# Optimization experiments

Measured on AMD Instinct MI355X. Metric: run time of the kernel, lower is better.

Reference implementation:

```python
import jax, jax.numpy as jnp
import numpy as np

DILATIONS = (1, 2, 4, 8, 16, 32, 64, 128, 256)
R = 128          # residual/skip channels
K = 3            # kernel size
B, CIN, T = 8, 1, 16384
COUT = 1
L = len(DILATIONS)


def causal_conv(x, w, b, dilation):
    # x: [B, Cin, T], w: [Cout, Cin, K] -> [B, Cout, T], left-padded (causal)
    k = w.shape[-1]
    pad = dilation * (k - 1)
    y = jax.lax.conv_general_dilated(
        x, w, window_strides=(1,), padding=[(pad, 0)],
        rhs_dilation=(dilation,), dimension_numbers=("NCH", "OIH", "NCH"))
    return y + b[None, :, None]


def setup_inputs() -> dict:
    key = jax.random.key(0)
    ks = jax.random.split(key, 11)
    s = 0.1  # weight scale to keep gated activations in a healthy range
    return {
        "x": jax.random.normal(ks[0], (B, CIN, T), jnp.float32),
        "input_w": s * jax.random.normal(ks[1], (R, CIN, 1), jnp.float32),
        "input_b": s * jax.random.normal(ks[2], (R,), jnp.float32),
        "conv_w": s * jax.random.normal(ks[3], (L, 2 * R, R, K), jnp.float32),
        "conv_b": s * jax.random.normal(ks[4], (L, 2 * R), jnp.float32),
        "out_w": s * jax.random.normal(ks[5], (L, R, R, 1), jnp.float32),
        "out_b": s * jax.random.normal(ks[6], (L, R), jnp.float32),
        "output1_w": s * jax.random.normal(ks[7], (R, R * L, 1), jnp.float32),
        "output1_b": s * jax.random.normal(ks[8], (R,), jnp.float32),
        "output2_w": s * jax.random.normal(ks[9], (COUT, R, 1), jnp.float32),
        "output2_b": s * jax.random.normal(ks[10], (COUT,), jnp.float32),
    }


def reference(x, input_w, input_b, conv_w, conv_b, out_w, out_b,
              output1_w, output1_b, output2_w, output2_b):
    # input layer: 1x1 conv + tanh (use_output_transform=False)
    h = jnp.tanh(causal_conv(x, input_w, input_b, 1))

    skips = []
    for i, d in enumerate(DILATIONS):
        pre = causal_conv(h, conv_w[i], conv_b[i], d)      # [B, 2R, T]
        t, g = jnp.split(pre, 2, axis=1)
        z = jnp.tanh(t) * jax.nn.sigmoid(g)                # gated activation
        skips.append(z)                                     # skip = activation out
        res = causal_conv(z, out_w[i], out_b[i], 1)         # 1x1 output transform
        h = h + res                                         # residual connection

    sk = jnp.concatenate(skips, axis=1)                     # [B, R*L, T]
    y = jnp.tanh(causal_conv(sk, output1_w, output1_b, 1))
    out = causal_conv(y, output2_w, output2_b, 1)           # linear
    return out
```

## Files before the change

kernel.cpp:

```cpp
#include <hip/hip_runtime.h>
#include <cstdint>
#include <cstddef>

#define T_LEN 16384
#define BATCH 8
#define NLAYER 9

typedef _Float16 f16;
typedef __attribute__((ext_vector_type(8))) _Float16 f16x8;
typedef __attribute__((ext_vector_type(4))) float f32x4;
#define MFMA_F16 __builtin_amdgcn_mfma_f32_16x16x32_f16

__device__ __forceinline__ float fast_sigmoid(float x) {
    return 1.0f / (1.0f + __expf(-x));
}
__device__ __forceinline__ float fast_tanh(float x) {
    return 1.0f - 2.0f / (__expf(2.0f * x) + 1.0f);
}

__global__ __launch_bounds__(256) void prep_weights(
    const float* __restrict__ cw, const float* __restrict__ ow,
    const float* __restrict__ o1w, f16* __restrict__ wA, f16* __restrict__ wB)
{
    int n = blockIdx.x * 256 + threadIdx.x;
    const int NA = NLAYER * 12 * 256 * 32;
    const int NB = NLAYER * 4 * 256 * 32;
    if (n < NA) {
        int kp = n & 31; int q = n >> 5;
        int c = q & 255; q >>= 8;
        int ch = q % 12; int l = q / 12;
        int tap = ch >> 2;
        int r = (ch & 3) * 32 + kp;
        wA[n] = (f16)cw[((size_t)(l * 256 + c) * 128 + r) * 3 + tap];
    } else if (n < NA + NB) {
        int m = n - NA;
        int kp = m & 31; int q = m >> 5;
        int c = q & 255; q >>= 8;
        int ch = q & 3; int l = q >> 2;
        int k = ch * 32 + kp;
        float v = (c < 128) ? ow[(size_t)(l * 128 + c) * 128 + k]
                            : o1w[(size_t)(c - 128) * 1152 + l * 128 + k];
        wB[m] = (f16)v;
    }
}

__global__ __launch_bounds__(256) void input_init(
    const float* __restrict__ x, const float* __restrict__ iw,
    const float* __restrict__ ib,
    f16* __restrict__ h, f16* __restrict__ acc1)
{
    int n = blockIdx.x * 256 + threadIdx.x;
    int r = n & 127; int bt = n >> 7;
    h[n] = (f16)fast_tanh(iw[r] * x[bt] + ib[r]);
    acc1[n] = (f16)0.0f;
}

__global__ __launch_bounds__(256, 3) void layer_kernel(
    const f16* __restrict__ h_in, f16* __restrict__ h_out,
    f16* __restrict__ acc1,
    const f16* __restrict__ wA,
    const f16* __restrict__ wB,
    const float* __restrict__ cb,
    const float* __restrict__ ob,
    int d)
{
    __shared__ __align__(16) f16 Bs[2][256 * 32];
    __shared__ __align__(16) f16 zs[64][136];

    const int tid  = threadIdx.x;
    const int lane = tid & 63;
    const int w4   = tid >> 6;
    const int mg   = w4 & 1;
    const int ng   = w4 >> 1;
    const int col  = lane & 15;
    const int quad = lane >> 4;
    const int b    = blockIdx.y;
    const int t0   = blockIdx.x * 64;

    const f16* hb = h_in + (size_t)b * T_LEN * 128;

    f32x4 acc[2][8];
#pragma unroll
    for (int mt = 0; mt < 2; ++mt)
#pragma unroll
        for (int nt = 0; nt < 8; ++nt) acc[mt][nt] = (f32x4)0.0f;

    f16x8 sv[4];
    {
        const f16* src = wA;
#pragma unroll
        for (int i = 0; i < 4; ++i) sv[i] = *(const f16x8*)&src[tid * 32 + i * 8];
#pragma unroll
        for (int i = 0; i < 4; ++i) *(f16x8*)&Bs[0][tid * 32 + i * 8] = sv[i];
    }
    __syncthreads();

#pragma unroll
    for (int ch = 0; ch < 12; ++ch) {
        if (ch < 11) {
            const f16* src = wA + (ch + 1) * (256 * 32);
#pragma unroll
            for (int i = 0; i < 4; ++i) sv[i] = *(const f16x8*)&src[tid * 32 + i * 8];
        }
        const int tap = ch >> 2;
        const int off = (2 - tap) * d;
        const int kb  = (ch & 3) * 32 + quad * 8;
        const f16* bsc = &Bs[ch & 1][0];
        f16x8 a[2];
#pragma unroll
        for (int mt = 0; mt < 2; ++mt) {
            int t = t0 + mg * 32 + mt * 16 + col - off;
            if (t >= 0) a[mt] = *(const f16x8*)&hb[(size_t)t * 128 + kb];
            else        a[mt] = (f16x8)(f16)0.0f;
        }
#pragma unroll
        for (int nt = 0; nt < 8; ++nt) {
            int nb = (nt < 4) ? (ng * 64 + nt * 16) : (128 + ng * 64 + (nt - 4) * 16);
            f16x8 bf = *(const f16x8*)&bsc[(nb + col) * 32 + quad * 8];
            acc[0][nt] = MFMA_F16(a[0], bf, acc[0][nt], 0, 0, 0);
            acc[1][nt] = MFMA_F16(a[1], bf, acc[1][nt], 0, 0, 0);
        }
        if (ch < 11) {
#pragma unroll
            for (int i = 0; i < 4; ++i)
                *(f16x8*)&Bs[(ch + 1) & 1][tid * 32 + i * 8] = sv[i];
        }
        __syncthreads();
    }

#pragma unroll
    for (int nt = 0; nt < 4; ++nt) {
        int j = ng * 64 + nt * 16 + col;
        float cf = cb[j];
        float cg = cb[j + 128];
#pragma unroll
        for (int mt = 0; mt < 2; ++mt)
#pragma unroll
            for (int reg = 0; reg < 4; ++reg) {
                float f = acc[mt][nt][reg]     + cf;
                float g = acc[mt][nt + 4][reg] + cg;
                zs[mg * 32 + mt * 16 + quad * 4 + reg][j] =
                    (f16)(fast_tanh(f) * fast_sigmoid(g));
            }
    }
    {
        const f16* src = wB;
#pragma unroll
        for (int i = 0; i < 4; ++i) sv[i] = *(const f16x8*)&src[tid * 32 + i * 8];
#pragma unroll
        for (int i = 0; i < 4; ++i) *(f16x8*)&Bs[0][tid * 32 + i * 8] = sv[i];
    }
    __syncthreads();

    f32x4 acc2[2][8];
#pragma unroll
    for (int mt = 0; mt < 2; ++mt)
#pragma unroll
        for (int nt = 0; nt < 8; ++nt) acc2[mt][nt] = (f32x4)0.0f;

#pragma unroll
    for (int ch = 0; ch < 4; ++ch) {
        if (ch < 3) {
            const f16* src = wB + (ch + 1) * (256 * 32);
#pragma unroll
            for (int i = 0; i < 4; ++i) sv[i] = *(const f16x8*)&src[tid * 32 + i * 8];
        }
        const f16* bsc = &Bs[ch & 1][0];
        f16x8 a[2];
#pragma unroll
        for (int mt = 0; mt < 2; ++mt)
            a[mt] = *(const f16x8*)&zs[mg * 32 + mt * 16 + col][ch * 32 + quad * 8];
#pragma unroll
        for (int nt = 0; nt < 8; ++nt) {
            int nb = (nt < 4) ? (ng * 64 + nt * 16) : (128 + ng * 64 + (nt - 4) * 16);
            f16x8 bf = *(const f16x8*)&bsc[(nb + col) * 32 + quad * 8];
            acc2[0][nt] = MFMA_F16(a[0], bf, acc2[0][nt], 0, 0, 0);
            acc2[1][nt] = MFMA_F16(a[1], bf, acc2[1][nt], 0, 0, 0);
        }
        if (ch < 3) {
#pragma unroll
            for (int i = 0; i < 4; ++i)
                *(f16x8*)&Bs[(ch + 1) & 1][tid * 32 + i * 8] = sv[i];
        }
        __syncthreads();
    }

#pragma unroll
    for (int nt = 0; nt < 4; ++nt) {
        int n = ng * 64 + nt * 16 + col;
        float o = ob[n];
#pragma unroll
        for (int mt = 0; mt < 2; ++mt)
#pragma unroll
            for (int reg = 0; reg < 4; ++reg)
                zs[mg * 32 + mt * 16 + quad * 4 + reg][n] =
                    (f16)(acc2[mt][nt][reg] + o);
    }
    __syncthreads();
    const int orow = tid >> 2, oseg = tid & 3;
    const size_t gb = (size_t)b * T_LEN * 128 + (size_t)(t0 + orow) * 128 + oseg * 32;
#pragma unroll
    for (int i = 0; i < 4; ++i) {
        f16x8 rv = *(const f16x8*)&zs[orow][oseg * 32 + i * 8];
        f16x8 hv = *(const f16x8*)&h_in[gb + i * 8];
        *(f16x8*)&h_out[gb + i * 8] = hv + rv;
    }
    __syncthreads();

#pragma unroll
    for (int nt = 0; nt < 4; ++nt) {
        int n = ng * 64 + nt * 16 + col;
#pragma unroll
        for (int mt = 0; mt < 2; ++mt)
#pragma unroll
            for (int reg = 0; reg < 4; ++reg)
                zs[mg * 32 + mt * 16 + quad * 4 + reg][n] = (f16)acc2[mt][nt + 4][reg];
    }
    __syncthreads();
#pragma unroll
    for (int i = 0; i < 4; ++i) {
        f16x8 sv2 = *(const f16x8*)&zs[orow][oseg * 32 + i * 8];
        f16x8 av  = *(const f16x8*)&acc1[gb + i * 8];
        *(f16x8*)&acc1[gb + i * 8] = av + sv2;
    }
}

__global__ __launch_bounds__(256) void final_kernel(
    const f16* __restrict__ acc1, const float* __restrict__ b1,
    const float* __restrict__ w2, const float* __restrict__ b2,
    float* __restrict__ out)
{
    int lane = threadIdx.x & 63;
    int w = threadIdx.x >> 6;
    int bt = blockIdx.x * 4 + w;
    float v0 = (float)acc1[(size_t)bt * 128 + lane];
    float v1 = (float)acc1[(size_t)bt * 128 + lane + 64];
    float s = w2[lane] * fast_tanh(v0 + b1[lane]) +
              w2[lane + 64] * fast_tanh(v1 + b1[lane + 64]);
#pragma unroll
    for (int k = 1; k < 64; k <<= 1) s += __shfl_xor(s, k, 64);
    if (lane == 0) out[bt] = s + b2[0];
}

extern "C" void kernel_launch(void* const* d_in, const int* in_sizes, int n_in,
                              void* d_out, int out_size, void* d_ws, size_t ws_size,
                              hipStream_t stream)
{
    const float* x   = (const float*)d_in[0];
    const float* iw  = (const float*)d_in[1];
    const float* ib  = (const float*)d_in[2];
    const float* cw  = (const float*)d_in[3];
    const float* cb  = (const float*)d_in[4];
    const float* ow  = (const float*)d_in[5];
    const float* ob  = (const float*)d_in[6];
    const float* o1w = (const float*)d_in[7];
    const float* o1b = (const float*)d_in[8];
    const float* o2w = (const float*)d_in[9];
    const float* o2b = (const float*)d_in[10];
    float* out = (float*)d_out;

    const size_t HTR = (size_t)BATCH * T_LEN * 128;
    f16* hA   = (f16*)d_ws;
    f16* hB   = hA + HTR;
    f16* acc1 = hB + HTR;
    f16* wAp  = acc1 + HTR;
    f16* wBp  = wAp + (size_t)NLAYER * 12 * 256 * 32;

    prep_weights<<<4608, 256, 0, stream>>>(cw, ow, o1w, wAp, wBp);
    input_init<<<65536, 256, 0, stream>>>(x, iw, ib, hA, acc1);

    const int DIL[NLAYER] = {1, 2, 4, 8, 16, 32, 64, 128, 256};
    f16* hin = hA; f16* hout = hB;
    for (int l = 0; l < NLAYER; ++l) {
        layer_kernel<<<dim3(T_LEN / 64, BATCH), 256, 0, stream>>>(
            hin, hout, acc1,
            wAp + (size_t)l * 12 * 256 * 32, wBp + (size_t)l * 4 * 256 * 32,
            cb + l * 256, ob + l * 128, DIL[l]);
        f16* tmp = hin; hin = hout; hout = tmp;
    }
    final_kernel<<<BATCH * T_LEN / 4, 256, 0, stream>>>(acc1, o1b, o2w, o2b, out);
}
```

Measured before the change: 870.0 us.

## Double time tile per block, swizzle weight LDS, read 1x1 weights from global

```diff
diff --git a/kernel.cpp b/kernel.cpp
--- a/kernel.cpp
+++ b/kernel.cpp
@@ -55,7 +55,7 @@
     acc1[n] = (f16)0.0f;
 }
 
-__global__ __launch_bounds__(256, 3) void layer_kernel(
+__global__ __launch_bounds__(256, 2) void layer_kernel(
     const f16* __restrict__ h_in, f16* __restrict__ h_out,
     f16* __restrict__ acc1,
     const f16* __restrict__ wA,
@@ -64,8 +64,9 @@
     const float* __restrict__ ob,
     int d)
 {
-    __shared__ __align__(16) f16 Bs[2][256 * 32];
-    __shared__ __align__(16) f16 zs[64][136];
+    __shared__ __align__(16) char smem_raw[34816];
+    f16* const Bsm = (f16*)smem_raw;
+    f16* const zs  = (f16*)smem_raw;
 
     const int tid  = threadIdx.x;
     const int lane = tid & 63;
@@ -75,55 +76,61 @@
     const int col  = lane & 15;
     const int quad = lane >> 4;
     const int b    = blockIdx.y;
-    const int t0   = blockIdx.x * 64;
+    const int t0   = blockIdx.x * 128;
 
     const f16* hb = h_in + (size_t)b * T_LEN * 128;
 
-    f32x4 acc[2][8];
-#pragma unroll
-    for (int mt = 0; mt < 2; ++mt)
+    const int bswz = (quad ^ ((col >> 1) & 3)) * 8;
+    const int wsw  = (tid >> 1) & 3;
+
+    f32x4 acc[4][8];
+#pragma unroll
+    for (int mt = 0; mt < 4; ++mt)
 #pragma unroll
         for (int nt = 0; nt < 8; ++nt) acc[mt][nt] = (f32x4)0.0f;
 
     f16x8 sv[4];
     {
-        const f16* src = wA;
-#pragma unroll
-        for (int i = 0; i < 4; ++i) sv[i] = *(const f16x8*)&src[tid * 32 + i * 8];
-#pragma unroll
-        for (int i = 0; i < 4; ++i) *(f16x8*)&Bs[0][tid * 32 + i * 8] = sv[i];
+        const f16* src = wA + tid * 32;
+#pragma unroll
+        for (int i = 0; i < 4; ++i) sv[i] = *(const f16x8*)&src[i * 8];
+#pragma unroll
+        for (int i = 0; i < 4; ++i)
+            *(f16x8*)&Bsm[tid * 32 + ((i ^ wsw) * 8)] = sv[i];
     }
     __syncthreads();
 
 #pragma unroll
     for (int ch = 0; ch < 12; ++ch) {
         if (ch < 11) {
-            const f16* src = wA + (ch + 1) * (256 * 32);
-#pragma unroll
-            for (int i = 0; i < 4; ++i) sv[i] = *(const f16x8*)&src[tid * 32 + i * 8];
+            const f16* src = wA + (ch + 1) * 8192 + tid * 32;
+#pragma unroll
+            for (int i = 0; i < 4; ++i) sv[i] = *(const f16x8*)&src[i * 8];
         }
         const int tap = ch >> 2;
         const int off = (2 - tap) * d;
         const int kb  = (ch & 3) * 32 + quad * 8;
-        const f16* bsc = &Bs[ch & 1][0];
-        f16x8 a[2];
-#pragma unroll
-        for (int mt = 0; mt < 2; ++mt) {
-            int t = t0 + mg * 32 + mt * 16 + col - off;
+        f16x8 a[4];
+#pragma unroll
+        for (int mt = 0; mt < 4; ++mt) {
+            int t = t0 + mg * 64 + mt * 16 + col - off;
             if (t >= 0) a[mt] = *(const f16x8*)&hb[(size_t)t * 128 + kb];
             else        a[mt] = (f16x8)(f16)0.0f;
         }
+        const f16* bsc = Bsm + (ch & 1) * 8192;
 #pragma unroll
         for (int nt = 0; nt < 8; ++nt) {
             int nb = (nt < 4) ? (ng * 64 + nt * 16) : (128 + ng * 64 + (nt - 4) * 16);
-            f16x8 bf = *(const f16x8*)&bsc[(nb + col) * 32 + quad * 8];
+            f16x8 bf = *(const f16x8*)&bsc[(nb + col) * 32 + bswz];
             acc[0][nt] = MFMA_F16(a[0], bf, acc[0][nt], 0, 0, 0);
             acc[1][nt] = MFMA_F16(a[1], bf, acc[1][nt], 0, 0, 0);
+            acc[2][nt] = MFMA_F16(a[2], bf, acc[2][nt], 0, 0, 0);
+            acc[3][nt] = MFMA_F16(a[3], bf, acc[3][nt], 0, 0, 0);
         }
         if (ch < 11) {
-#pragma unroll
-            for (int i = 0; i < 4; ++i)
-                *(f16x8*)&Bs[(ch + 1) & 1][tid * 32 + i * 8] = sv[i];
+            f16* dst = Bsm + ((ch + 1) & 1) * 8192 + tid * 32;
+#pragma unroll
+            for (int i = 0; i < 4; ++i) *(f16x8*)&dst[(i ^ wsw) * 8] = sv[i];
         }
         __syncthreads();
     }
@@ -134,74 +141,58 @@
         float cf = cb[j];
         float cg = cb[j + 128];
 #pragma unroll
-        for (int mt = 0; mt < 2; ++mt)
+        for (int mt = 0; mt < 4; ++mt)
 #pragma unroll
             for (int reg = 0; reg < 4; ++reg) {
                 float f = acc[mt][nt][reg]     + cf;
                 float g = acc[mt][nt + 4][reg] + cg;
-                zs[mg * 32 + mt * 16 + quad * 4 + reg][j] =
+                zs[(mg * 64 + mt * 16 + quad * 4 + reg) * 136 + j] =
                     (f16)(fast_tanh(f) * fast_sigmoid(g));
             }
     }
-    {
-        const f16* src = wB;
-#pragma unroll
-        for (int i = 0; i < 4; ++i) sv[i] = *(const f16x8*)&src[tid * 32 + i * 8];
-#pragma unroll
-        for (int i = 0; i < 4; ++i) *(f16x8*)&Bs[0][tid * 32 + i * 8] = sv[i];
-    }
-    __syncthreads();
-
-    f32x4 acc2[2][8];
-#pragma unroll
-    for (int mt = 0; mt < 2; ++mt)
-#pragma unroll
-        for (int nt = 0; nt < 8; ++nt) acc2[mt][nt] = (f32x4)0.0f;
+    __syncthreads();
+
+#pragma unroll
+    for (int mt = 0; mt < 4; ++mt)
+#pragma unroll
+        for (int nt = 0; nt < 8; ++nt) acc[mt][nt] = (f32x4)0.0f;
 
 #pragma unroll
     for (int ch = 0; ch < 4; ++ch) {
-        if (ch < 3) {
-            const f16* src = wB + (ch + 1) * (256 * 32);
-#pragma unroll
-            for (int i = 0; i < 4; ++i) sv[i] = *(const f16x8*)&src[tid * 32 + i * 8];
-        }
-        const f16* bsc = &Bs[ch & 1][0];
-        f16x8 a[2];
-#pragma unroll
-        for (int mt = 0; mt < 2; ++mt)
-            a[mt] = *(const f16x8*)&zs[mg * 32 + mt * 16 + col][ch * 32 + quad * 8];
+        f16x8 a[4];
+#pragma unroll
+        for (int mt = 0; mt < 4; ++mt)
+            a[mt] = *(const f16x8*)&zs[(mg * 64 + mt * 16 + col) * 136 + ch * 32 + quad * 8];
+        const f16* wc = wB + ch * 8192;
 #pragma unroll
         for (int nt = 0; nt < 8; ++nt) {
             int nb = (nt < 4) ? (ng * 64 + nt * 16) : (128 + ng * 64 + (nt - 4) * 16);
-            f16x8 bf = *(const f16x8*)&bsc[(nb + col) * 32 + quad * 8];
-            acc2[0][nt] = MFMA_F16(a[0], bf, acc2[0][nt], 0, 0, 0);
-            acc2[1][nt] = MFMA_F16(a[1], bf, acc2[1][nt], 0, 0, 0);
-        }
-        if (ch < 3) {
-#pragma unroll
-            for (int i = 0; i < 4; ++i)
-                *(f16x8*)&Bs[(ch + 1) & 1][tid * 32 + i * 8] = sv[i];
-        }
-        __syncthreads();
-    }
+            f16x8 bf = *(const f16x8*)&wc[(nb + col) * 32 + quad * 8];
+            acc[0][nt] = MFMA_F16(a[0], bf, acc[0][nt], 0, 0, 0);
+            acc[1][nt] = MFMA_F16(a[1], bf, acc[1][nt], 0, 0, 0);
+            acc[2][nt] = MFMA_F16(a[2], bf, acc[2][nt], 0, 0, 0);
+            acc[3][nt] = MFMA_F16(a[3], bf, acc[3][nt], 0, 0, 0);
+        }
+    }
+    __syncthreads();
 
 #pragma unroll
     for (int nt = 0; nt < 4; ++nt) {
         int n = ng * 64 + nt * 16 + col;
         float o = ob[n];
 #pragma unroll
-        for (int mt = 0; mt < 2; ++mt)
+        for (int mt = 0; mt < 4; ++mt)
 #pragma unroll
             for (int reg = 0; reg < 4; ++reg)
-                zs[mg * 32 + mt * 16 + quad * 4 + reg][n] =
-                    (f16)(acc2[mt][nt][reg] + o);
-    }
-    __syncthreads();
-    const int orow = tid >> 2, oseg = tid & 3;
-    const size_t gb = (size_t)b * T_LEN * 128 + (size_t)(t0 + orow) * 128 + oseg * 32;
-#pragma unroll
-    for (int i = 0; i < 4; ++i) {
-        f16x8 rv = *(const f16x8*)&zs[orow][oseg * 32 + i * 8];
+                zs[(mg * 64 + mt * 16 + quad * 4 + reg) * 136 + n] =
+                    (f16)(acc[mt][nt][reg] + o);
+    }
+    __syncthreads();
+    const int orow = tid >> 1, oseg = tid & 1;
+    const size_t gb = (size_t)b * T_LEN * 128 + (size_t)(t0 + orow) * 128 + oseg * 64;
+#pragma unroll
+    for (int i = 0; i < 8; ++i) {
+        f16x8 rv = *(const f16x8*)&zs[orow * 136 + oseg * 64 + i * 8];
         f16x8 hv = *(const f16x8*)&h_in[gb + i * 8];
         *(f16x8*)&h_out[gb + i * 8] = hv + rv;
     }
@@ -211,15 +202,16 @@
     for (int nt = 0; nt < 4; ++nt) {
         int n = ng * 64 + nt * 16 + col;
 #pragma unroll
-        for (int mt = 0; mt < 2; ++mt)
+        for (int mt = 0; mt < 4; ++mt)
 #pragma unroll
             for (int reg = 0; reg < 4; ++reg)
-                zs[mg * 32 + mt * 16 + quad * 4 + reg][n] = (f16)acc2[mt][nt + 4][reg];
-    }
-    __syncthreads();
-#pragma unroll
-    for (int i = 0; i < 4; ++i) {
-        f16x8 sv2 = *(const f16x8*)&zs[orow][oseg * 32 + i * 8];
+                zs[(mg * 64 + mt * 16 + quad * 4 + reg) * 136 + n] =
+                    (f16)acc[mt][nt + 4][reg];
+    }
+    __syncthreads();
+#pragma unroll
+    for (int i = 0; i < 8; ++i) {
+        f16x8 sv2 = *(const f16x8*)&zs[orow * 136 + oseg * 64 + i * 8];
         f16x8 av  = *(const f16x8*)&acc1[gb + i * 8];
         *(f16x8*)&acc1[gb + i * 8] = av + sv2;
     }
@@ -272,7 +264,7 @@
     const int DIL[NLAYER] = {1, 2, 4, 8, 16, 32, 64, 128, 256};
     f16* hin = hA; f16* hout = hB;
     for (int l = 0; l < NLAYER; ++l) {
-        layer_kernel<<<dim3(T_LEN / 64, BATCH), 256, 0, stream>>>(
+        layer_kernel<<<dim3(T_LEN / 128, BATCH), 256, 0, stream>>>(
             hin, hout, acc1,
             wAp + (size_t)l * 12 * 256 * 32, wBp + (size_t)l * 4 * 256 * 32,
             cb + l * 256, ob + l * 128, DIL[l]);
```

Result: slower. 913.9 us (+5.1%).
